# Optimization experiments

Hardware: AMD Instinct MI355X
Metric: run time of the kernel (lower is better)

Reference implementation:

```python
import jax, jax.numpy as jnp
import numpy as np

GRID_SIZE = 5
SPLINE_ORDER = 3
GRID_RANGE = (-1.0, 1.0)
EPS = 1e-8


def _make_grid():
    h = (GRID_RANGE[1] - GRID_RANGE[0]) / GRID_SIZE
    # knots: [-spline_order, ..., grid_size + spline_order] * h + lo  -> 12 values
    return jnp.arange(-SPLINE_ORDER, GRID_SIZE + SPLINE_ORDER + 1, dtype=jnp.float32) * h + GRID_RANGE[0]


def _bspline_basis(x, grid):
    # x: [N, in]  ->  bases: [N, in, num_basis] with num_basis = grid_size + spline_order
    xe = x[..., None]                                   # [N, in, 1]
    bases = ((xe >= grid[:-1]) & (xe < grid[1:])).astype(x.dtype)  # [N, in, 11]
    for k in range(1, SPLINE_ORDER + 1):
        left = (xe - grid[: -(k + 1)]) / (grid[k:-1] - grid[: -(k + 1)] + EPS) * bases[..., :-1]
        right = (grid[k + 1:] - xe) / (grid[k + 1:] - grid[1:-k] + EPS) * bases[..., 1:]
        bases = left + right
    return bases                                        # [N, in, 8]


def setup_inputs() -> dict:
    key = jax.random.key(0)
    k1, k2, k3 = jax.random.split(key, 3)
    in_f, out_f, num_basis = 1024, 1024, GRID_SIZE + SPLINE_ORDER
    N = 4096
    x = jax.random.normal(k1, (N, in_f), dtype=jnp.float32)
    base_weight = jax.random.normal(k2, (out_f, in_f), dtype=jnp.float32) * (1.0 / np.sqrt(in_f))
    base_bias = jnp.zeros((out_f,), dtype=jnp.float32)
    spline_weight = jax.random.normal(k3, (out_f, in_f, num_basis), dtype=jnp.float32) * (1.0 / np.sqrt(in_f))
    return {"x": x, "base_weight": base_weight, "base_bias": base_bias, "spline_weight": spline_weight}


def reference(x, base_weight, base_bias, spline_weight):
    grid = _make_grid()
    # base path: SiLU(x) @ W_base^T + b
    base_out = jax.nn.silu(x) @ base_weight.T + base_bias          # [N, out]
    # spline path: Cox-de Boor basis then contraction over (in, basis)
    basis = _bspline_basis(x, grid)                                 # [N, in, 8]
    spline_out = jnp.einsum('nib,oib->no', basis, spline_weight)    # [N, out]
    return base_out + spline_out
```

## Files before the change

kernel.cpp:

```cpp
#include <hip/hip_runtime.h>
#include <hip/hip_bf16.h>
#include <stdint.h>

#define IN_F 1024
#define OUT_F 1024
#define NB 8
#define KDIM (IN_F + IN_F * NB)
#define NROWS 4096
#define SLICE_ELEMS (NROWS * OUT_F)
#define PREP_BLOCKS ((NROWS * IN_F) / 256)
#define WCONV_BLOCKS ((OUT_F * KDIM) / (4 * 256))

typedef __attribute__((ext_vector_type(8))) short bf16x8;
typedef __attribute__((ext_vector_type(4))) short bf16x4;
typedef __attribute__((ext_vector_type(4))) float f32x4;

__device__ __forceinline__ void bspline8(float x, float b8[8]) {
  float u = (x + 2.2f) * 2.5f;
  bool in = (u >= 0.0f) && (u < 11.0f);
  float uc = fminf(fmaxf(u, 0.0f), 10.99f);
  int i = (int)uc;
  float f = uc - (float)i;
  float g = 1.0f - f;
  float f2 = f * f, f3 = f2 * f;
  const float s = 1.0f / 6.0f;
  float v0 = f3 * s;
  float v1 = (-3.0f * f3 + 3.0f * f2 + 3.0f * f + 1.0f) * s;
  float v2 = (3.0f * f3 - 6.0f * f2 + 4.0f) * s;
  float v3 = g * g * g * s;
#pragma unroll
  for (int j = 0; j < 8; ++j) {
    int d = i - j;
    float r = (d == 0) ? v0 : (d == 1) ? v1 : (d == 2) ? v2 : (d == 3) ? v3 : 0.0f;
    b8[j] = in ? r : 0.0f;
  }
}

__global__ void prep_all_kernel(const float* __restrict__ x, const float* __restrict__ bw,
                                const float* __restrict__ sw, __hip_bfloat16* __restrict__ A,
                                __hip_bfloat16* __restrict__ W) {
  if (blockIdx.x < PREP_BLOCKS) {
    int idx = blockIdx.x * 256 + threadIdx.x;
    int n = idx >> 10;
    int i = idx & 1023;
    float xv = x[idx];
    float sl = xv / (1.0f + __expf(-xv));
    __hip_bfloat16* row = A + (size_t)n * KDIM;
    row[i] = __float2bfloat16(sl);
    float b8[8];
    bspline8(xv, b8);
    alignas(16) __hip_bfloat16 tmp[8];
#pragma unroll
    for (int c = 0; c < 8; ++c) tmp[c] = __float2bfloat16(b8[c]);
    *(bf16x8*)(row + IN_F + i * 8) = *(const bf16x8*)tmp;
  } else {
    int v = (blockIdx.x - PREP_BLOCKS) * 256 + threadIdx.x;
    int e = v * 4;
    int o = e / KDIM;
    int k = e - o * KDIM;
    float4 val = (k < IN_F) ? *(const float4*)(bw + o * IN_F + k)
                            : *(const float4*)(sw + (size_t)o * (IN_F * NB) + (k - IN_F));
    alignas(8) __hip_bfloat16 t[4];
    t[0] = __float2bfloat16(val.x);
    t[1] = __float2bfloat16(val.y);
    t[2] = __float2bfloat16(val.z);
    t[3] = __float2bfloat16(val.w);
    *(bf16x4*)(W + e) = *(const bf16x4*)t;
  }
}

__global__ __launch_bounds__(512, 2) void gemm8_kernel(const __hip_bfloat16* __restrict__ A,
                                                       const __hip_bfloat16* __restrict__ W,
                                                       float* __restrict__ dst,
                                                       const float* __restrict__ bias,
                                                       int kslice, int use_bias) {
  __shared__ __hip_bfloat16 lA[2][16384];
  __shared__ __hip_bfloat16 lB[2][16384];
  const int tid = threadIdx.x;
  const int wave = tid >> 6;
  const int lane = tid & 63;
  const int warp_m = wave >> 2;
  const int warp_n = wave & 3;
  const int bm = blockIdx.x * 256;
  const int bn = blockIdx.y * 256;
  const int z = blockIdx.z;
  float* __restrict__ d = dst + (size_t)z * SLICE_ELEMS;
  const int kbeg = z * kslice;
  const int NT = kslice >> 6;
  const int srow = lane & 15;
  const int skc = (lane >> 4) * 8;
  const int r = lane & 15;
  const int quad = lane >> 4;

  const __hip_bfloat16* rowA[2];
  const __hip_bfloat16* rowB[2];
  rowA[0] = A + (size_t)(bm + (0 * 8 + wave) * 16 + srow) * KDIM + kbeg + skc;
  rowA[1] = A + (size_t)(bm + (1 * 8 + wave) * 16 + srow) * KDIM + kbeg + skc;
  rowB[0] = W + (size_t)(bn + (0 * 8 + wave) * 16 + srow) * KDIM + kbeg + skc;
  rowB[1] = W + (size_t)(bn + (1 * 8 + wave) * 16 + srow) * KDIM + kbeg + skc;

  f32x4 acc[8][4];
#pragma unroll
  for (int a = 0; a < 8; ++a)
#pragma unroll
    for (int b = 0; b < 4; ++b) acc[a][b] = (f32x4){0.f, 0.f, 0.f, 0.f};

#define GLOAD(SRC, DST)                                                                      \
  __builtin_amdgcn_global_load_lds((const __attribute__((address_space(1))) void*)(SRC),     \
                                   (__attribute__((address_space(3))) void*)(DST), 16, 0, 0)

#define STAGE_HALF(TILE, HID, SLOT)                                              \
  do {                                                                           \
    const int tu_ = (TILE);                                                      \
    const int ts_ = tu_ < NT ? tu_ : NT - 1;                                     \
    if ((HID) < 2) {                                                             \
      const __hip_bfloat16* s_ = rowA[(HID)] + (size_t)ts_ * 64;                 \
      __hip_bfloat16* d_ = &lA[(SLOT)][(((HID) * 8 + wave) * 2 + 0) * 512];      \
      GLOAD(s_, d_);                                                             \
      GLOAD(s_ + 32, d_ + 512);                                                  \
    } else {                                                                     \
      const __hip_bfloat16* s_ = rowB[(HID) - 2] + (size_t)ts_ * 64;             \
      __hip_bfloat16* d_ = &lB[(SLOT)][((((HID) - 2) * 8 + wave) * 2 + 0) * 512];\
      GLOAD(s_, d_);                                                             \
      GLOAD(s_ + 32, d_ + 512);                                                  \
    }                                                                            \
  } while (0)

  bf16x8 a03[4][2], a47[4][2], bfr[4][2];

#define LOAD_A03(SLOT)                                                                      \
  do {                                                                                      \
    _Pragma("unroll") for (int t = 0; t < 4; ++t) {                                         \
      a03[t][0] = *(const bf16x8*)&lA[(SLOT)][((warp_m * 8 + t) * 2 + 0) * 512 + lane * 8]; \
      a03[t][1] = *(const bf16x8*)&lA[(SLOT)][((warp_m * 8 + t) * 2 + 1) * 512 + lane * 8]; \
    }                                                                                       \
  } while (0)
#define LOAD_A47(SLOT)                                                                          \
  do {                                                                                          \
    _Pragma("unroll") for (int t = 0; t < 4; ++t) {                                             \
      a47[t][0] = *(const bf16x8*)&lA[(SLOT)][((warp_m * 8 + 4 + t) * 2 + 0) * 512 + lane * 8]; \
      a47[t][1] = *(const bf16x8*)&lA[(SLOT)][((warp_m * 8 + 4 + t) * 2 + 1) * 512 + lane * 8]; \
    }                                                                                           \
  } while (0)
#define LOAD_B01(SLOT)                                                                      \
  do {                                                                                      \
    _Pragma("unroll") for (int u = 0; u < 2; ++u) {                                         \
      bfr[u][0] = *(const bf16x8*)&lB[(SLOT)][((warp_n * 4 + u) * 2 + 0) * 512 + lane * 8]; \
      bfr[u][1] = *(const bf16x8*)&lB[(SLOT)][((warp_n * 4 + u) * 2 + 1) * 512 + lane * 8]; \
    }                                                                                       \
  } while (0)
#define LOAD_B23(SLOT)                                                                          \
  do {                                                                                          \
    _Pragma("unroll") for (int u = 0; u < 2; ++u) {                                             \
      bfr[2 + u][0] =                                                                           \
          *(const bf16x8*)&lB[(SLOT)][((warp_n * 4 + 2 + u) * 2 + 0) * 512 + lane * 8];         \
      bfr[2 + u][1] =                                                                           \
          *(const bf16x8*)&lB[(SLOT)][((warp_n * 4 + 2 + u) * 2 + 1) * 512 + lane * 8];         \
    }                                                                                           \
  } while (0)

#define MFMA_QUAD(AF, TM0, TN0)                                                              \
  do {                                                                                       \
    _Pragma("unroll") for (int tm = 0; tm < 4; ++tm)                                         \
    _Pragma("unroll") for (int tn = 0; tn < 2; ++tn)                                         \
    _Pragma("unroll") for (int s = 0; s < 2; ++s)                                            \
        acc[(TM0) + tm][(TN0) + tn] = __builtin_amdgcn_mfma_f32_16x16x32_bf16(               \
            AF[tm][s], bfr[(TN0) + tn][s], acc[(TM0) + tm][(TN0) + tn], 0, 0, 0);            \
  } while (0)

#define PIN() __builtin_amdgcn_sched_barrier(0)

  STAGE_HALF(0, 0, 0);
  STAGE_HALF(0, 1, 0);
  STAGE_HALF(0, 2, 0);
  STAGE_HALF(0, 3, 0);
  STAGE_HALF(1, 0, 1);
  STAGE_HALF(1, 1, 1);
  STAGE_HALF(1, 2, 1);
  STAGE_HALF(1, 3, 1);
  asm volatile("s_waitcnt vmcnt(8)" ::: "memory");
  PIN();
  __builtin_amdgcn_s_barrier();
  LOAD_A03(0);
  LOAD_B01(0);
  PIN();

  for (int it = 0; it < NT; ++it) {
    const int p = it & 1;
    LOAD_A47(p);
    PIN();
    __builtin_amdgcn_s_setprio(1);
    MFMA_QUAD(a03, 0, 0);
    __builtin_amdgcn_s_setprio(0);
    PIN();
    __builtin_amdgcn_s_barrier();
    LOAD_B23(p);
    PIN();
    __builtin_amdgcn_s_setprio(1);
    MFMA_QUAD(a47, 4, 0);
    __builtin_amdgcn_s_setprio(0);
    PIN();
    __builtin_amdgcn_s_barrier();
    STAGE_HALF(it + 2, 0, p);
    STAGE_HALF(it + 2, 1, p);
    PIN();
    __builtin_amdgcn_s_setprio(1);
    MFMA_QUAD(a03, 0, 2);
    __builtin_amdgcn_s_setprio(0);
    PIN();
    __builtin_amdgcn_s_barrier();
    STAGE_HALF(it + 2, 2, p);
    STAGE_HALF(it + 2, 3, p);
    asm volatile("s_waitcnt vmcnt(8)" ::: "memory");
    PIN();
    __builtin_amdgcn_s_barrier();
    LOAD_A03(p ^ 1);
    LOAD_B01(p ^ 1);
    PIN();
    __builtin_amdgcn_s_setprio(1);
    MFMA_QUAD(a47, 4, 2);
    __builtin_amdgcn_s_setprio(0);
    PIN();
    __builtin_amdgcn_s_barrier();
  }
  asm volatile("s_waitcnt vmcnt(0)" ::: "memory");

#undef STAGE_HALF
#undef GLOAD
#undef LOAD_A03
#undef LOAD_A47
#undef LOAD_B01
#undef LOAD_B23
#undef MFMA_QUAD
#undef PIN

#pragma unroll
  for (int tm = 0; tm < 8; ++tm) {
#pragma unroll
    for (int tn = 0; tn < 4; ++tn) {
      const int col = bn + warp_n * 64 + tn * 16 + r;
      const float bv = use_bias ? bias[col] : 0.0f;
#pragma unroll
      for (int reg = 0; reg < 4; ++reg) {
        const int rowi = bm + warp_m * 128 + tm * 16 + quad * 4 + reg;
        d[(size_t)rowi * OUT_F + col] = acc[tm][tn][reg] + bv;
      }
    }
  }
}

__global__ void reduce_kernel(const float* __restrict__ P, const float* __restrict__ bias,
                              float* __restrict__ out, int S) {
  int v = blockIdx.x * 256 + threadIdx.x;
  int e = v * 4;
  int o = e & (OUT_F - 1);
  float4 acc = *(const float4*)(bias + o);
  for (int s = 0; s < S; ++s) {
    float4 p = *(const float4*)(P + (size_t)s * SLICE_ELEMS + e);
    acc.x += p.x;
    acc.y += p.y;
    acc.z += p.z;
    acc.w += p.w;
  }
  *(float4*)(out + e) = acc;
}

__global__ void kan_fallback(const float* __restrict__ x, const float* __restrict__ bw,
                             const float* __restrict__ bb, const float* __restrict__ sw,
                             float* __restrict__ out) {
  __shared__ float act[KDIM];
  int n = blockIdx.x;
  for (int i = threadIdx.x; i < IN_F; i += 256) {
    float xv = x[(size_t)n * IN_F + i];
    act[i] = xv / (1.0f + __expf(-xv));
    float b8[8];
    bspline8(xv, b8);
#pragma unroll
    for (int c = 0; c < 8; ++c) act[IN_F + i * 8 + c] = b8[c];
  }
  __syncthreads();
  for (int o = threadIdx.x; o < OUT_F; o += 256) {
    float s = bb[o];
    const float* wbp = bw + (size_t)o * IN_F;
    for (int k = 0; k < IN_F; ++k) s += act[k] * wbp[k];
    const float* wsp = sw + (size_t)o * (IN_F * NB);
    for (int k = 0; k < IN_F * NB; ++k) s += act[IN_F + k] * wsp[k];
    out[(size_t)n * OUT_F + o] = s;
  }
}

extern "C" void kernel_launch(void* const* d_in, const int* in_sizes, int n_in, void* d_out,
                              int out_size, void* d_ws, size_t ws_size, hipStream_t stream) {
  const float* x = (const float*)d_in[0];
  const float* bw = (const float*)d_in[1];
  const float* bb = (const float*)d_in[2];
  const float* sw = (const float*)d_in[3];
  float* out = (float*)d_out;

  const size_t needA = (size_t)NROWS * KDIM * 2;
  const size_t needW = (size_t)OUT_F * KDIM * 2;
  const size_t sliceB = (size_t)SLICE_ELEMS * 4;
  if (ws_size < needA + needW) {
    kan_fallback<<<NROWS, 256, 0, stream>>>(x, bw, bb, sw, out);
    return;
  }
  __hip_bfloat16* A = (__hip_bfloat16*)d_ws;
  __hip_bfloat16* W = (__hip_bfloat16*)((char*)d_ws + needA);
  float* P = (float*)((char*)d_ws + needA + needW);
  const size_t avail = ws_size - needA - needW;
  int S = (avail >= 4 * sliceB) ? 4 : (avail >= 2 * sliceB) ? 2 : 1;

  prep_all_kernel<<<PREP_BLOCKS + WCONV_BLOCKS, 256, 0, stream>>>(x, bw, sw, A, W);
  if (S == 1) {
    gemm8_kernel<<<dim3(NROWS / 256, OUT_F / 256, 1), 512, 0, stream>>>(A, W, out, bb, KDIM, 1);
  } else {
    gemm8_kernel<<<dim3(NROWS / 256, OUT_F / 256, S), 512, 0, stream>>>(A, W, P, bb, KDIM / S, 0);
    reduce_kernel<<<SLICE_ELEMS / (4 * 256), 256, 0, stream>>>(P, bb, out, S);
  }
}
```

Measured before the change: 244.1 us.

## Reorder GEMM phase schedule with split B fragments and 2x unrolled main loop

Splits the B fragment registers into two halves (b01/b23) so B and A sub-tiles can be loaded in a different phase order. The per-tile pipeline now loads A03, A47 and B23 ahead of their MFMA groups with explicit lgkmcnt waits and barriers. The main loop is unrolled by two so the LDS slot index is a compile-time constant. The new ordering adds more barriers and explicit LDS waits per tile, which may reduce overlap. It also assumes NT is even, or tiles will be skipped.

```diff
diff --git a/kernel.cpp b/kernel.cpp
--- a/kernel.cpp
+++ b/kernel.cpp
@@ -84,9 +84,11 @@
   const int bm = blockIdx.x * 256;
   const int bn = blockIdx.y * 256;
   const int z = blockIdx.z;
+
   float* __restrict__ d = dst + (size_t)z * SLICE_ELEMS;
   const int kbeg = z * kslice;
   const int NT = kslice >> 6;
+  const int NIT = NT >> 1;
   const int srow = lane & 15;
   const int skc = (lane >> 4) * 8;
   const int r = lane & 15;
@@ -126,7 +128,7 @@
     }                                                                            \
   } while (0)
 
-  bf16x8 a03[4][2], a47[4][2], bfr[4][2];
+  bf16x8 a03[4][2], a47[4][2], b01[2][2], b23[2][2];
 
 #define LOAD_A03(SLOT)                                                                      \
   do {                                                                                      \
@@ -145,86 +147,102 @@
 #define LOAD_B01(SLOT)                                                                      \
   do {                                                                                      \
     _Pragma("unroll") for (int u = 0; u < 2; ++u) {                                         \
-      bfr[u][0] = *(const bf16x8*)&lB[(SLOT)][((warp_n * 4 + u) * 2 + 0) * 512 + lane * 8]; \
-      bfr[u][1] = *(const bf16x8*)&lB[(SLOT)][((warp_n * 4 + u) * 2 + 1) * 512 + lane * 8]; \
+      b01[u][0] = *(const bf16x8*)&lB[(SLOT)][((warp_n * 4 + u) * 2 + 0) * 512 + lane * 8]; \
+      b01[u][1] = *(const bf16x8*)&lB[(SLOT)][((warp_n * 4 + u) * 2 + 1) * 512 + lane * 8]; \
     }                                                                                       \
   } while (0)
 #define LOAD_B23(SLOT)                                                                          \
   do {                                                                                          \
     _Pragma("unroll") for (int u = 0; u < 2; ++u) {                                             \
-      bfr[2 + u][0] =                                                                           \
+      b23[u][0] =                                                                               \
           *(const bf16x8*)&lB[(SLOT)][((warp_n * 4 + 2 + u) * 2 + 0) * 512 + lane * 8];         \
-      bfr[2 + u][1] =                                                                           \
+      b23[u][1] =                                                                               \
           *(const bf16x8*)&lB[(SLOT)][((warp_n * 4 + 2 + u) * 2 + 1) * 512 + lane * 8];         \
     }                                                                                           \
   } while (0)
 
-#define MFMA_QUAD(AF, TM0, TN0)                                                              \
+#define MFMA_QUAD(AF, BF, TM0, TN0)                                                          \
   do {                                                                                       \
     _Pragma("unroll") for (int tm = 0; tm < 4; ++tm)                                         \
     _Pragma("unroll") for (int tn = 0; tn < 2; ++tn)                                         \
     _Pragma("unroll") for (int s = 0; s < 2; ++s)                                            \
         acc[(TM0) + tm][(TN0) + tn] = __builtin_amdgcn_mfma_f32_16x16x32_bf16(               \
-            AF[tm][s], bfr[(TN0) + tn][s], acc[(TM0) + tm][(TN0) + tn], 0, 0, 0);            \
+            AF[tm][s], BF[tn][s], acc[(TM0) + tm][(TN0) + tn], 0, 0, 0);                     \
   } while (0)
 
 #define PIN() __builtin_amdgcn_sched_barrier(0)
-
+#define PH_BAR_LGKM()                                        \
+  do {                                                       \
+    __builtin_amdgcn_s_barrier();                            \
+    asm volatile("s_waitcnt lgkmcnt(0)" ::: "memory");       \
+    PIN();                                                   \
+  } while (0)
+#define PH_END()                                             \
+  do {                                                       \
+    __builtin_amdgcn_s_setprio(0);                           \
+    PIN();                                                   \
+    __builtin_amdgcn_s_barrier();                            \
+  } while (0)
+
+#define TILE_BODY(P, T2)                                         \
+  do {                                                           \
+              \
+    LOAD_A03(P);                                                 \
+    PH_BAR_LGKM();                                               \
+    __builtin_amdgcn_s_setprio(1);                               \
+    MFMA_QUAD(a03, b01, 0, 0);                                   \
+    PH_END();                                                    \
+                             \
+    LOAD_A47(P);                                                 \
+    PH_BAR_LGKM();                                               \
+    __builtin_amdgcn_s_setprio(1);                               \
+    MFMA_QUAD(a47, b01, 4, 0);                                   \
+    PH_END();                                                    \
+      \
+    LOAD_B23(P);                                                 \
+    STAGE_HALF(T2, 0, P);                                        \
+    STAGE_HALF(T2, 1, P);                                        \
+    PH_BAR_LGKM();                                               \
+    __builtin_amdgcn_s_setprio(1);                               \
+    MFMA_QUAD(a47, b23, 4, 2);                                   \
+    PH_END();                                                    \
+    \
+    \
+                                             \
+    STAGE_HALF(T2, 2, P);                                        \
+    STAGE_HALF(T2, 3, P);                                        \
+    asm volatile("s_waitcnt vmcnt(8)" ::: "memory");             \
+    PIN();                                                       \
+    __builtin_amdgcn_s_barrier();                                \
+    PIN();                                                       \
+    LOAD_B01((P) ^ 1);                                           \
+    __builtin_amdgcn_s_setprio(1);                               \
+    MFMA_QUAD(a03, b23, 0, 2);                                   \
+    PH_END();                                                    \
+  } while (0)
+
+  STAGE_HALF(0, 2, 0);
+  STAGE_HALF(0, 3, 0);
   STAGE_HALF(0, 0, 0);
   STAGE_HALF(0, 1, 0);
-  STAGE_HALF(0, 2, 0);
-  STAGE_HALF(0, 3, 0);
+  STAGE_HALF(1, 2, 1);
+  STAGE_HALF(1, 3, 1);
   STAGE_HALF(1, 0, 1);
   STAGE_HALF(1, 1, 1);
-  STAGE_HALF(1, 2, 1);
-  STAGE_HALF(1, 3, 1);
   asm volatile("s_waitcnt vmcnt(8)" ::: "memory");
   PIN();
   __builtin_amdgcn_s_barrier();
-  LOAD_A03(0);
+  PIN();
   LOAD_B01(0);
   PIN();
 
-  for (int it = 0; it < NT; ++it) {
-    const int p = it & 1;
-    LOAD_A47(p);
-    PIN();
-    __builtin_amdgcn_s_setprio(1);
-    MFMA_QUAD(a03, 0, 0);
-    __builtin_amdgcn_s_setprio(0);
-    PIN();
-    __builtin_amdgcn_s_barrier();
-    LOAD_B23(p);
-    PIN();
-    __builtin_amdgcn_s_setprio(1);
-    MFMA_QUAD(a47, 4, 0);
-    __builtin_amdgcn_s_setprio(0);
-    PIN();
-    __builtin_amdgcn_s_barrier();
-    STAGE_HALF(it + 2, 0, p);
-    STAGE_HALF(it + 2, 1, p);
-    PIN();
-    __builtin_amdgcn_s_setprio(1);
-    MFMA_QUAD(a03, 0, 2);
-    __builtin_amdgcn_s_setprio(0);
-    PIN();
-    __builtin_amdgcn_s_barrier();
-    STAGE_HALF(it + 2, 2, p);
-    STAGE_HALF(it + 2, 3, p);
-    asm volatile("s_waitcnt vmcnt(8)" ::: "memory");
-    PIN();
-    __builtin_amdgcn_s_barrier();
-    LOAD_A03(p ^ 1);
-    LOAD_B01(p ^ 1);
-    PIN();
-    __builtin_amdgcn_s_setprio(1);
-    MFMA_QUAD(a47, 4, 2);
-    __builtin_amdgcn_s_setprio(0);
-    PIN();
-    __builtin_amdgcn_s_barrier();
+  for (int i = 0; i < NIT; ++i) {
+    TILE_BODY(0, 2 * i + 2);
+    TILE_BODY(1, 2 * i + 3);
   }
   asm volatile("s_waitcnt vmcnt(0)" ::: "memory");
 
+#undef TILE_BODY
 #undef STAGE_HALF
 #undef GLOAD
 #undef LOAD_A03
@@ -232,6 +250,8 @@
 #undef LOAD_B01
 #undef LOAD_B23
 #undef MFMA_QUAD
+#undef PH_BAR_LGKM
+#undef PH_END
 #undef PIN
 
 #pragma unroll
```

New measurement: 232.2 us. -4.9%, faster.
